# Optimization experiments

Hardware: AMD Instinct MI355X
Metric: run time of the kernel (lower is better)

## Reference

```python
import jax, jax.numpy as jnp
import numpy as np

TEMPERATURE = 0.05
EPS = 1e-8  # F.cosine_similarity default eps


def setup_inputs() -> dict:
    key = jax.random.key(0)
    k1, k2 = jax.random.split(key)
    N, D = 8192, 256
    return {
        "query_embeddings": jax.random.normal(k1, (N, D), dtype=jnp.float32),
        "pos_embeddings": jax.random.normal(k2, (N, D), dtype=jnp.float32),
    }


def _normalize(x):
    # matches F.cosine_similarity: x / max(||x||, eps)
    norm = jnp.sqrt(jnp.sum(x * x, axis=-1, keepdims=True))
    return x / jnp.maximum(norm, EPS)


def reference(query_embeddings, pos_embeddings):
    q = _normalize(query_embeddings)  # [N, D]
    p = _normalize(pos_embeddings)    # [N, D]
    # cosine similarity matrix via GEMM instead of (N,N,D) broadcast
    sim = jnp.einsum("nd,md->nm", q, p) / TEMPERATURE  # [N, N]
    # cross-entropy with labels = arange(N): loss_i = logsumexp(sim_i) - sim_ii
    logz = jax.nn.logsumexp(sim, axis=-1)  # [N]
    diag = jnp.diagonal(sim)               # [N]
    loss = jnp.mean(logz - diag)
    return loss
```

## Files before the change

### kernel.cpp

```cpp
#include <hip/hip_runtime.h>
#include <hip/hip_bf16.h>

#define NROWS 8192
#define DDIM  256
#define INV_TEMP 20.0f

typedef __attribute__((ext_vector_type(8))) short bf16x8;
typedef __attribute__((ext_vector_type(4))) float f32x4;

__device__ static inline void async16(const void* g, void* l) {
    __builtin_amdgcn_global_load_lds(
        (const __attribute__((address_space(1))) void*)g,
        (__attribute__((address_space(3))) void*)l, 16, 0, 0);
}

__global__ __launch_bounds__(64) void norm_diag_kernel(
    const float* __restrict__ q, const float* __restrict__ p,
    unsigned short* __restrict__ qn, unsigned short* __restrict__ pn,
    float* __restrict__ diag)
{
    const int row  = blockIdx.x;
    const int lane = threadIdx.x;

    const float4 qv = ((const float4*)(q + (size_t)row * DDIM))[lane];
    const float4 pv = ((const float4*)(p + (size_t)row * DDIM))[lane];

    float sq = qv.x*qv.x + qv.y*qv.y + qv.z*qv.z + qv.w*qv.w;
    float sp = pv.x*pv.x + pv.y*pv.y + pv.z*pv.z + pv.w*pv.w;
    #pragma unroll
    for (int m = 1; m < 64; m <<= 1) {
        sq += __shfl_xor(sq, m);
        sp += __shfl_xor(sp, m);
    }
    const float qs = 1.0f / fmaxf(sqrtf(sq), 1e-8f);
    const float ps = 1.0f / fmaxf(sqrtf(sp), 1e-8f);

    const float qx = qv.x*qs, qy = qv.y*qs, qz = qv.z*qs, qw = qv.w*qs;
    const float px = pv.x*ps, py = pv.y*ps, pz = pv.z*ps, pw = pv.w*ps;

    float d = qx*px + qy*py + qz*pz + qw*pw;
    #pragma unroll
    for (int m = 1; m < 64; m <<= 1) d += __shfl_xor(d, m);
    if (lane == 0) diag[row] = d * INV_TEMP;

    union { unsigned short u16[4]; uint2 v; } uq, up;
    {
        __hip_bfloat16 b;
        b = __float2bfloat16(qx); uq.u16[0] = *(unsigned short*)&b;
        b = __float2bfloat16(qy); uq.u16[1] = *(unsigned short*)&b;
        b = __float2bfloat16(qz); uq.u16[2] = *(unsigned short*)&b;
        b = __float2bfloat16(qw); uq.u16[3] = *(unsigned short*)&b;
        b = __float2bfloat16(px); up.u16[0] = *(unsigned short*)&b;
        b = __float2bfloat16(py); up.u16[1] = *(unsigned short*)&b;
        b = __float2bfloat16(pz); up.u16[2] = *(unsigned short*)&b;
        b = __float2bfloat16(pw); up.u16[3] = *(unsigned short*)&b;
    }
    *(uint2*)(qn + (size_t)row * DDIM + lane * 4) = uq.v;
    *(uint2*)(pn + (size_t)row * DDIM + lane * 4) = up.v;
}

__global__ __launch_bounds__(256, 2) void simexp_kernel(
    const unsigned short* __restrict__ qn,
    const unsigned short* __restrict__ pn,
    float* __restrict__ part)
{
    __shared__ unsigned char lds[16384];

    const int tid  = threadIdx.x;
    const int lane = tid & 63;
    const int w    = tid >> 6;
    const int wr   = w >> 1;
    const int wc   = w & 1;
    const int quad = lane >> 4;
    const int l16  = lane & 15;
    const int rowbase = blockIdx.y * 128;
    const int colbase = blockIdx.x * 128;

    const unsigned short* gA0 = qn + (size_t)(rowbase + (2*w  )*16 + l16) * DDIM + quad * 8;
    const unsigned short* gA1 = qn + (size_t)(rowbase + (2*w+1)*16 + l16) * DDIM + quad * 8;
    const unsigned short* gB0 = pn + (size_t)(colbase + (2*w  )*16 + l16) * DDIM + quad * 8;
    const unsigned short* gB1 = pn + (size_t)(colbase + (2*w+1)*16 + l16) * DDIM + quad * 8;

    unsigned char* ldsA = lds;
    unsigned char* ldsB = lds + 8192;

    f32x4 acc[4][4];
    #pragma unroll
    for (int i = 0; i < 4; ++i)
        #pragma unroll
        for (int j = 0; j < 4; ++j) acc[i][j] = (f32x4)0.0f;

    for (int ks = 0; ks < 8; ++ks) {
        __syncthreads();
        async16(gA0 + ks * 32, ldsA + (2*w    ) * 1024);
        async16(gA1 + ks * 32, ldsA + (2*w + 1) * 1024);
        async16(gB0 + ks * 32, ldsB + (2*w    ) * 1024);
        async16(gB1 + ks * 32, ldsB + (2*w + 1) * 1024);
        __syncthreads();

        bf16x8 af[4], bf[4];
        #pragma unroll
        for (int i = 0; i < 4; ++i)
            af[i] = *(const bf16x8*)(ldsA + (wr*4 + i) * 1024 + quad * 256 + l16 * 16);
        #pragma unroll
        for (int j = 0; j < 4; ++j)
            bf[j] = *(const bf16x8*)(ldsB + (wc*4 + j) * 1024 + quad * 256 + l16 * 16);

        #pragma unroll
        for (int i = 0; i < 4; ++i)
            #pragma unroll
            for (int j = 0; j < 4; ++j)
                acc[i][j] = __builtin_amdgcn_mfma_f32_16x16x32_bf16(
                    af[i], bf[j], acc[i][j], 0, 0, 0);
    }

    __syncthreads();
    float* red = (float*)lds;

    #pragma unroll
    for (int i = 0; i < 4; ++i)
        #pragma unroll
        for (int r = 0; r < 4; ++r) {
            float s = __expf(acc[i][0][r] * INV_TEMP)
                    + __expf(acc[i][1][r] * INV_TEMP)
                    + __expf(acc[i][2][r] * INV_TEMP)
                    + __expf(acc[i][3][r] * INV_TEMP);
            s += __shfl_xor(s, 1);
            s += __shfl_xor(s, 2);
            s += __shfl_xor(s, 4);
            s += __shfl_xor(s, 8);
            if (l16 == 0)
                red[wc * 128 + wr * 64 + i * 16 + quad * 4 + r] = s;
        }
    __syncthreads();

    if (tid < 128)
        part[(size_t)blockIdx.x * NROWS + rowbase + tid] = red[tid] + red[128 + tid];
}

__global__ __launch_bounds__(128) void rowsum_kernel(
    const float* __restrict__ part, const float* __restrict__ diag,
    float* __restrict__ loss_part)
{
    const int row = blockIdx.x * 128 + threadIdx.x;
    float s = 0.0f;
    #pragma unroll 4
    for (int cb = 0; cb < 64; ++cb)
        s += part[(size_t)cb * NROWS + row];
    float v = logf(s) - diag[row];

    #pragma unroll
    for (int m = 1; m < 64; m <<= 1) v += __shfl_xor(v, m);
    __shared__ float wsum[2];
    if ((threadIdx.x & 63) == 0) wsum[threadIdx.x >> 6] = v;
    __syncthreads();
    if (threadIdx.x == 0) loss_part[blockIdx.x] = wsum[0] + wsum[1];
}

__global__ __launch_bounds__(64) void final_kernel(
    const float* __restrict__ loss_part, float* __restrict__ out)
{
    float v = loss_part[threadIdx.x];
    #pragma unroll
    for (int m = 1; m < 64; m <<= 1) v += __shfl_xor(v, m);
    if (threadIdx.x == 0) out[0] = v * (1.0f / NROWS);
}

extern "C" void kernel_launch(void* const* d_in, const int* in_sizes, int n_in,
                              void* d_out, int out_size, void* d_ws, size_t ws_size,
                              hipStream_t stream)
{
    const float* q = (const float*)d_in[0];
    const float* p = (const float*)d_in[1];

    char* ws = (char*)d_ws;
    unsigned short* qn   = (unsigned short*)ws;
    unsigned short* pn   = (unsigned short*)(ws + (size_t)NROWS*DDIM*2);
    float* part      = (float*)(ws + 2*(size_t)NROWS*DDIM*2);
    float* diag      = part + 64 * (size_t)NROWS;
    float* loss_part = diag + NROWS;

    norm_diag_kernel<<<NROWS, 64, 0, stream>>>(q, p, qn, pn, diag);

    dim3 grid(64, 64);
    simexp_kernel<<<grid, 256, 0, stream>>>(qn, pn, part);

    rowsum_kernel<<<64, 128, 0, stream>>>(part, diag, loss_part);
    final_kernel<<<1, 64, 0, stream>>>(loss_part, (float*)d_out);
}
```

Before: 147.2 us.

## Double-buffer GEMM K-tiles, atomically accumulate row sums, and merge reduction kernels

The similarity GEMM now stages 64-wide K chunks into two 32 KB LDS buffers, prefetching the next chunk while MFMAs run on the current one, with one barrier per iteration instead of two. Per-block partial exp-sums are added straight into a per-row global array with atomicAdd, which removes the 2 MB partial buffer and the rowsum kernel. A single 1024-thread final kernel computes the log and mean. The norm kernel handles four rows per block and zero-initializes the accumulator. In exchange, 64 KB of LDS per block may limit occupancy, the atomics may contend, and the summation order is no longer deterministic.

```diff
diff --git a/kernel.cpp b/kernel.cpp
--- a/kernel.cpp
+++ b/kernel.cpp
@@ -14,13 +14,13 @@
         (__attribute__((address_space(3))) void*)l, 16, 0, 0);
 }
 
-__global__ __launch_bounds__(64) void norm_diag_kernel(
+__global__ __launch_bounds__(256) void norm_diag_kernel(
     const float* __restrict__ q, const float* __restrict__ p,
     unsigned short* __restrict__ qn, unsigned short* __restrict__ pn,
-    float* __restrict__ diag)
+    float* __restrict__ diag, float* __restrict__ lse)
 {
-    const int row  = blockIdx.x;
-    const int lane = threadIdx.x;
+    const int row  = blockIdx.x * 4 + (threadIdx.x >> 6);
+    const int lane = threadIdx.x & 63;
 
     const float4 qv = ((const float4*)(q + (size_t)row * DDIM))[lane];
     const float4 pv = ((const float4*)(p + (size_t)row * DDIM))[lane];
@@ -41,7 +41,10 @@
     float d = qx*px + qy*py + qz*pz + qw*pw;
     #pragma unroll
     for (int m = 1; m < 64; m <<= 1) d += __shfl_xor(d, m);
-    if (lane == 0) diag[row] = d * INV_TEMP;
+    if (lane == 0) {
+        diag[row] = d * INV_TEMP;
+        lse[row]  = 0.0f;
+    }
 
     union { unsigned short u16[4]; uint2 v; } uq, up;
     {
@@ -62,9 +65,9 @@
 __global__ __launch_bounds__(256, 2) void simexp_kernel(
     const unsigned short* __restrict__ qn,
     const unsigned short* __restrict__ pn,
-    float* __restrict__ part)
+    float* __restrict__ lse)
 {
-    __shared__ unsigned char lds[16384];
+    __shared__ unsigned char lds[65536];
 
     const int tid  = threadIdx.x;
     const int lane = tid & 63;
@@ -76,13 +79,10 @@
     const int rowbase = blockIdx.y * 128;
     const int colbase = blockIdx.x * 128;
 
-    const unsigned short* gA0 = qn + (size_t)(rowbase + (2*w  )*16 + l16) * DDIM + quad * 8;
-    const unsigned short* gA1 = qn + (size_t)(rowbase + (2*w+1)*16 + l16) * DDIM + quad * 8;
-    const unsigned short* gB0 = pn + (size_t)(colbase + (2*w  )*16 + l16) * DDIM + quad * 8;
-    const unsigned short* gB1 = pn + (size_t)(colbase + (2*w+1)*16 + l16) * DDIM + quad * 8;
-
-    unsigned char* ldsA = lds;
-    unsigned char* ldsB = lds + 8192;
+    const unsigned short* sA0 = qn + (size_t)(rowbase + (2*w  )*16 + l16) * DDIM + quad * 8;
+    const unsigned short* sA1 = qn + (size_t)(rowbase + (2*w+1)*16 + l16) * DDIM + quad * 8;
+    const unsigned short* sB0 = pn + (size_t)(colbase + (2*w  )*16 + l16) * DDIM + quad * 8;
+    const unsigned short* sB1 = pn + (size_t)(colbase + (2*w+1)*16 + l16) * DDIM + quad * 8;
 
     f32x4 acc[4][4];
     #pragma unroll
@@ -90,32 +90,47 @@
         #pragma unroll
         for (int j = 0; j < 4; ++j) acc[i][j] = (f32x4)0.0f;
 
-    for (int ks = 0; ks < 8; ++ks) {
+    #define STAGE(buf, ks)                                                    \
+        {                                                                     \
+            unsigned char* A_ = lds + (buf) * 32768;                          \
+            unsigned char* B_ = A_ + 16384;                                   \
+            _Pragma("unroll")                                                 \
+            for (int h = 0; h < 2; ++h) {                                     \
+                const int off = (ks) * 64 + h * 32;                           \
+                async16(sA0 + off, A_ + (4*w     + h) * 1024);                \
+                async16(sA1 + off, A_ + (4*w + 2 + h) * 1024);                \
+                async16(sB0 + off, B_ + (4*w     + h) * 1024);                \
+                async16(sB1 + off, B_ + (4*w + 2 + h) * 1024);                \
+            }                                                                 \
+        }
+
+    STAGE(0, 0);
+
+    for (int ks = 0; ks < 4; ++ks) {
         __syncthreads();
-        async16(gA0 + ks * 32, ldsA + (2*w    ) * 1024);
-        async16(gA1 + ks * 32, ldsA + (2*w + 1) * 1024);
-        async16(gB0 + ks * 32, ldsB + (2*w    ) * 1024);
-        async16(gB1 + ks * 32, ldsB + (2*w + 1) * 1024);
-        __syncthreads();
+        if (ks < 3) STAGE((ks + 1) & 1, ks + 1);
 
-        bf16x8 af[4], bf[4];
-        #pragma unroll
-        for (int i = 0; i < 4; ++i)
-            af[i] = *(const bf16x8*)(ldsA + (wr*4 + i) * 1024 + quad * 256 + l16 * 16);
-        #pragma unroll
-        for (int j = 0; j < 4; ++j)
-            bf[j] = *(const bf16x8*)(ldsB + (wc*4 + j) * 1024 + quad * 256 + l16 * 16);
+        unsigned char* A = lds + (ks & 1) * 32768;
+        unsigned char* B = A + 16384;
 
         #pragma unroll
-        for (int i = 0; i < 4; ++i)
+        for (int h = 0; h < 2; ++h) {
+            bf16x8 af[4], bf[4];
+            #pragma unroll
+            for (int i = 0; i < 4; ++i)
+                af[i] = *(const bf16x8*)(A + ((wr*4 + i)*2 + h) * 1024 + quad * 256 + l16 * 16);
             #pragma unroll
             for (int j = 0; j < 4; ++j)
-                acc[i][j] = __builtin_amdgcn_mfma_f32_16x16x32_bf16(
-                    af[i], bf[j], acc[i][j], 0, 0, 0);
+                bf[j] = *(const bf16x8*)(B + ((wc*4 + j)*2 + h) * 1024 + quad * 256 + l16 * 16);
+            #pragma unroll
+            for (int i = 0; i < 4; ++i)
+                #pragma unroll
+                for (int j = 0; j < 4; ++j)
+                    acc[i][j] = __builtin_amdgcn_mfma_f32_16x16x32_bf16(
+                        af[i], bf[j], acc[i][j], 0, 0, 0);
+        }
     }
-
-    __syncthreads();
-    float* red = (float*)lds;
+    #undef STAGE
 
     #pragma unroll
     for (int i = 0; i < 4; ++i)
@@ -130,40 +145,29 @@
             s += __shfl_xor(s, 4);
             s += __shfl_xor(s, 8);
             if (l16 == 0)
-                red[wc * 128 + wr * 64 + i * 16 + quad * 4 + r] = s;
+                atomicAdd(&lse[rowbase + wr * 64 + i * 16 + quad * 4 + r], s);
         }
-    __syncthreads();
-
-    if (tid < 128)
-        part[(size_t)blockIdx.x * NROWS + rowbase + tid] = red[tid] + red[128 + tid];
 }
 
-__global__ __launch_bounds__(128) void rowsum_kernel(
-    const float* __restrict__ part, const float* __restrict__ diag,
-    float* __restrict__ loss_part)
+__global__ __launch_bounds__(1024) void final_kernel(
+    const float* __restrict__ lse, const float* __restrict__ diag,
+    float* __restrict__ out)
 {
-    const int row = blockIdx.x * 128 + threadIdx.x;
     float s = 0.0f;
-    #pragma unroll 4
-    for (int cb = 0; cb < 64; ++cb)
-        s += part[(size_t)cb * NROWS + row];
-    float v = logf(s) - diag[row];
+    for (int i = threadIdx.x; i < NROWS; i += 1024)
+        s += logf(lse[i]) - diag[i];
+    #pragma unroll
+    for (int m = 1; m < 64; m <<= 1) s += __shfl_xor(s, m);
 
-    #pragma unroll
-    for (int m = 1; m < 64; m <<= 1) v += __shfl_xor(v, m);
-    __shared__ float wsum[2];
-    if ((threadIdx.x & 63) == 0) wsum[threadIdx.x >> 6] = v;
+    __shared__ float wsum[16];
+    if ((threadIdx.x & 63) == 0) wsum[threadIdx.x >> 6] = s;
     __syncthreads();
-    if (threadIdx.x == 0) loss_part[blockIdx.x] = wsum[0] + wsum[1];
-}
-
-__global__ __launch_bounds__(64) void final_kernel(
-    const float* __restrict__ loss_part, float* __restrict__ out)
-{
-    float v = loss_part[threadIdx.x];
-    #pragma unroll
-    for (int m = 1; m < 64; m <<= 1) v += __shfl_xor(v, m);
-    if (threadIdx.x == 0) out[0] = v * (1.0f / NROWS);
+    if (threadIdx.x < 16) {
+        float v = wsum[threadIdx.x];
+        #pragma unroll
+        for (int m = 1; m < 16; m <<= 1) v += __shfl_xor(v, m);
+        if (threadIdx.x == 0) out[0] = v * (1.0f / NROWS);
+    }
 }
 
 extern "C" void kernel_launch(void* const* d_in, const int* in_sizes, int n_in,
@@ -174,17 +178,15 @@
     const float* p = (const float*)d_in[1];
 
     char* ws = (char*)d_ws;
-    unsigned short* qn   = (unsigned short*)ws;
-    unsigned short* pn   = (unsigned short*)(ws + (size_t)NROWS*DDIM*2);
-    float* part      = (float*)(ws + 2*(size_t)NROWS*DDIM*2);
-    float* diag      = part + 64 * (size_t)NROWS;
-    float* loss_part = diag + NROWS;
+    unsigned short* qn = (unsigned short*)ws;
+    unsigned short* pn = (unsigned short*)(ws + (size_t)NROWS*DDIM*2);
+    float* diag = (float*)(ws + 2 * (size_t)NROWS * DDIM * 2);
+    float* lse  = diag + NROWS;
 
-    norm_diag_kernel<<<NROWS, 64, 0, stream>>>(q, p, qn, pn, diag);
+    norm_diag_kernel<<<NROWS / 4, 256, 0, stream>>>(q, p, qn, pn, diag, lse);
 
     dim3 grid(64, 64);
-    simexp_kernel<<<grid, 256, 0, stream>>>(qn, pn, part);
+    simexp_kernel<<<grid, 256, 0, stream>>>(qn, pn, lse);
 
-    rowsum_kernel<<<64, 128, 0, stream>>>(part, diag, loss_part);
-    final_kernel<<<1, 64, 0, stream>>>(loss_part, (float*)d_out);
+    final_kernel<<<1, 1024, 0, stream>>>(lse, diag, (float*)d_out);
 }
```

Result: slower. 203.7 us (+38.4%).
